# Kernel optimization log

Measured on AMD Instinct MI355X. Metric: run time of the kernel, lower is better.

Reference implementation:

```python
import jax, jax.numpy as jnp
import numpy as np

N_NODES = 100000
N_EDGES = 800000
IN_SIZE = 128
OUT_SIZE = 64
DEPTH = 2


def setup_inputs() -> dict:
    key = jax.random.key(0)
    k1, k2, k3, k4, k5 = jax.random.split(key, 5)
    data = jax.random.normal(k1, (N_NODES, IN_SIZE), dtype=jnp.float32)
    W = jax.random.normal(k2, (IN_SIZE, OUT_SIZE), dtype=jnp.float32) * (1.0 / np.sqrt(IN_SIZE))
    b = jax.random.normal(k3, (OUT_SIZE,), dtype=jnp.float32) * 0.01
    src_idx = jax.random.randint(k4, (N_EDGES,), 0, N_NODES, dtype=jnp.int64)
    tgt_idx = jnp.sort(jax.random.randint(k5, (N_EDGES,), 0, N_NODES, dtype=jnp.int64))
    return {"data": data, "W": W, "b": b, "src_idx": src_idx, "tgt_idx": tgt_idx}


def reference(data, W, b, src_idx, tgt_idx):
    # GCN(X,S) = relu( A_S^depth (X W + b) )
    out = data @ W + b  # [N, out_size]
    n = data.shape[0]
    # per-target edge counts (message_size); same every depth iteration
    counts = jax.ops.segment_sum(jnp.ones_like(tgt_idx, dtype=out.dtype), tgt_idx, num_segments=n)
    m = counts[tgt_idx][:, None]  # [E, 1], >= 1 wherever indexed
    for _ in range(DEPTH):
        # own/(m*(m+1)) summed over m edges of a node == own/(m+1);
        # plus sum of sources/(m+1): mean-style normalization
        msg = out[tgt_idx] / (m * (m + 1.0)) + out[src_idx] / (m + 1.0)
        out = jax.ops.segment_sum(msg, tgt_idx, num_segments=n)
    return jax.nn.relu(out)
```

## Files before the change

### kernel.cpp

```cpp
#include <hip/hip_runtime.h>

#define N_NODES 100000
#define N_EDGES 800000
#define IN_SIZE 128
#define OUT_SIZE 64

#define GEMM_BLOCKS 512
#define RP_BLOCKS   128
#define N_TILES     (N_NODES / 16)

typedef __attribute__((ext_vector_type(8))) short short8;
typedef __attribute__((ext_vector_type(4))) float f32x4;

__device__ __forceinline__ unsigned short f2bf(float x) {
    unsigned u = __float_as_uint(x);
    u += 0x7FFFu + ((u >> 16) & 1u);
    return (unsigned short)(u >> 16);
}
__device__ __forceinline__ unsigned pack2(float lo, float hi) {
    return (unsigned)f2bf(lo) | ((unsigned)f2bf(hi) << 16);
}
__device__ __forceinline__ float bflo(unsigned u) { return __uint_as_float(u << 16); }
__device__ __forceinline__ float bfhi(unsigned u) { return __uint_as_float(u & 0xFFFF0000u); }

__global__ __launch_bounds__(256) void gemm_rowptr_kernel(
    const float* __restrict__ data, const float* __restrict__ W,
    const float* __restrict__ b, const int* __restrict__ tgt,
    unsigned short* __restrict__ H, int* __restrict__ rowptr)
{
    if (blockIdx.x >= GEMM_BLOCKS) {
        int t = (int)(blockIdx.x - GEMM_BLOCKS) * 256 + (int)threadIdx.x;
        for (; t <= N_NODES; t += RP_BLOCKS * 256) {
            int lo = 0, hi = N_EDGES;
            while (lo < hi) {
                const int mid = (lo + hi) >> 1;
                if (tgt[mid] < t) lo = mid + 1; else hi = mid;
            }
            rowptr[t] = lo;
        }
        return;
    }

    __shared__ unsigned short Clds[4][16 * 72];

    const int tid  = threadIdx.x;
    const int lane = tid & 63;
    const int wv   = tid >> 6;
    const int quad = lane >> 4;
    const int col  = lane & 15;

    union U8 { short8 v; unsigned short u[8]; };

    short8 wb[4][4];
    #pragma unroll
    for (int kc = 0; kc < 4; ++kc) {
        #pragma unroll
        for (int nt = 0; nt < 4; ++nt) {
            U8 t;
            #pragma unroll
            for (int j = 0; j < 8; ++j) {
                const int k = kc * 32 + quad * 8 + j;
                t.u[j] = f2bf(W[k * OUT_SIZE + nt * 16 + col]);
            }
            wb[kc][nt] = t.v;
        }
    }
    float bcol[4];
    #pragma unroll
    for (int nt = 0; nt < 4; ++nt) bcol[nt] = b[nt * 16 + col];

    unsigned short* cl = Clds[wv];
    const int gw = blockIdx.x * 4 + wv;

    for (int tile = gw; tile < N_TILES; tile += GEMM_BLOCKS * 4) {
        const int r0 = tile * 16;
        const float* arow = data + (size_t)(r0 + col) * IN_SIZE + quad * 8;

        short8 af[4];
        #pragma unroll
        for (int kc = 0; kc < 4; ++kc) {
            const float4 x0 = *(const float4*)(arow + kc * 32);
            const float4 x1 = *(const float4*)(arow + kc * 32 + 4);
            U8 t;
            t.u[0] = f2bf(x0.x); t.u[1] = f2bf(x0.y);
            t.u[2] = f2bf(x0.z); t.u[3] = f2bf(x0.w);
            t.u[4] = f2bf(x1.x); t.u[5] = f2bf(x1.y);
            t.u[6] = f2bf(x1.z); t.u[7] = f2bf(x1.w);
            af[kc] = t.v;
        }

        f32x4 acc[4];
        #pragma unroll
        for (int nt = 0; nt < 4; ++nt) acc[nt] = (f32x4){0.f, 0.f, 0.f, 0.f};
        #pragma unroll
        for (int kc = 0; kc < 4; ++kc) {
            #pragma unroll
            for (int nt = 0; nt < 4; ++nt)
                acc[nt] = __builtin_amdgcn_mfma_f32_16x16x32_bf16(
                    af[kc], wb[kc][nt], acc[nt], 0, 0, 0);
        }

        #pragma unroll
        for (int nt = 0; nt < 4; ++nt) {
            #pragma unroll
            for (int r = 0; r < 4; ++r)
                cl[(quad * 4 + r) * 72 + nt * 16 + col] =
                    f2bf(acc[nt][r] + bcol[nt]);
        }
        #pragma unroll
        for (int p = 0; p < 2; ++p) {
            const int row = p * 8 + (lane >> 3);
            const int seg = lane & 7;
            const uint4 vv = *(const uint4*)(cl + row * 72 + seg * 8);
            *(uint4*)(H + (size_t)(r0 + row) * OUT_SIZE + seg * 8) = vv;
        }
    }
}

__device__ __forceinline__ void acc_add(float* a, const uint4 v) {
    a[0] += bflo(v.x); a[1] += bfhi(v.x);
    a[2] += bflo(v.y); a[3] += bfhi(v.y);
    a[4] += bflo(v.z); a[5] += bfhi(v.z);
    a[6] += bflo(v.w); a[7] += bfhi(v.w);
}
__device__ __forceinline__ void acc_fma(float* a, const uint4 v, const float m) {
    a[0] = fmaf(bflo(v.x), m, a[0]); a[1] = fmaf(bfhi(v.x), m, a[1]);
    a[2] = fmaf(bflo(v.y), m, a[2]); a[3] = fmaf(bfhi(v.y), m, a[3]);
    a[4] = fmaf(bflo(v.z), m, a[4]); a[5] = fmaf(bfhi(v.z), m, a[5]);
    a[6] = fmaf(bflo(v.w), m, a[6]); a[7] = fmaf(bfhi(v.w), m, a[7]);
}

template <bool FINAL>
__global__ __launch_bounds__(256) void prop_kernel(
    const unsigned short* __restrict__ in, void* __restrict__ outp,
    const int* __restrict__ rowptr, const int* __restrict__ src)
{
    const int tid   = threadIdx.x;
    const int lane  = tid & 63;
    const int s     = lane & 7;
    const int lbase = lane & 56;
    const int node  = blockIdx.x * 32 + (tid >> 3);

    const int start = rowptr[node];
    const int end   = rowptr[node + 1];
    const int deg   = end - start;

    const uint4* inq = (const uint4*)in;
    const uint4 ownq = inq[(size_t)node * 8 + s];

    float acc[8];
    #pragma unroll
    for (int k = 0; k < 8; ++k) acc[k] = 0.f;

    for (int base = start; base < end; base += 8) {
        const int li = base + s;
        const int sv = (li < end) ? src[li] : 0;
        int cm = end - base; cm = cm < 8 ? cm : 8;
        #pragma unroll
        for (int j0 = 0; j0 < 8; j0 += 4) {
            if (j0 < cm) {
                const int s0 = __shfl(sv, lbase + j0 + 0, 64);
                const int s1 = __shfl(sv, lbase + j0 + 1, 64);
                const int s2 = __shfl(sv, lbase + j0 + 2, 64);
                const int s3 = __shfl(sv, lbase + j0 + 3, 64);
                const float m1 = (j0 + 1 < cm) ? 1.f : 0.f;
                const float m2 = (j0 + 2 < cm) ? 1.f : 0.f;
                const float m3 = (j0 + 3 < cm) ? 1.f : 0.f;
                const uint4 v0 = inq[(size_t)s0 * 8 + s];
                const uint4 v1 = inq[(size_t)s1 * 8 + s];
                const uint4 v2 = inq[(size_t)s2 * 8 + s];
                const uint4 v3 = inq[(size_t)s3 * 8 + s];
                acc_add(acc, v0);
                acc_fma(acc, v1, m1);
                acc_fma(acc, v2, m2);
                acc_fma(acc, v3, m3);
            }
        }
    }

    float o[8];
    if (deg == 0) {
        #pragma unroll
        for (int k = 0; k < 8; ++k) o[k] = 0.f;
    } else {
        const float inv = 1.0f / (float)(deg + 1);
        float own[8];
        acc_add(acc, ownq);
        #pragma unroll
        for (int k = 0; k < 8; ++k) {
            o[k] = acc[k] * inv;
            if (FINAL) o[k] = fmaxf(o[k], 0.f);
        }
        (void)own;
    }

    if (FINAL) {
        float* out = (float*)outp;
        float4 lo, hi;
        lo.x = o[0]; lo.y = o[1]; lo.z = o[2]; lo.w = o[3];
        hi.x = o[4]; hi.y = o[5]; hi.z = o[6]; hi.w = o[7];
        *(float4*)(out + (size_t)node * OUT_SIZE + s * 8)     = lo;
        *(float4*)(out + (size_t)node * OUT_SIZE + s * 8 + 4) = hi;
    } else {
        uint4 pv;
        pv.x = pack2(o[0], o[1]);
        pv.y = pack2(o[2], o[3]);
        pv.z = pack2(o[4], o[5]);
        pv.w = pack2(o[6], o[7]);
        ((uint4*)outp)[(size_t)node * 8 + s] = pv;
    }
}

extern "C" void kernel_launch(void* const* d_in, const int* in_sizes, int n_in,
                              void* d_out, int out_size, void* d_ws, size_t ws_size,
                              hipStream_t stream)
{
    const float* data = (const float*)d_in[0];
    const float* W    = (const float*)d_in[1];
    const float* b    = (const float*)d_in[2];
    const int*   src  = (const int*)d_in[3];
    const int*   tgt  = (const int*)d_in[4];

    unsigned short* H0 = (unsigned short*)d_ws;
    unsigned short* H1 = H0 + (size_t)N_NODES * OUT_SIZE;
    int* rowptr        = (int*)(H1 + (size_t)N_NODES * OUT_SIZE);

    gemm_rowptr_kernel<<<GEMM_BLOCKS + RP_BLOCKS, 256, 0, stream>>>(
        data, W, b, tgt, H0, rowptr);
    prop_kernel<false><<<N_NODES / 32, 256, 0, stream>>>(H0, H1, rowptr, src);
    prop_kernel<true ><<<N_NODES / 32, 256, 0, stream>>>(H1, d_out, rowptr, src);
}
```

Baseline: 152.2 us.

## Split bf16 feature matrix into column planes for cache-friendly gather

```diff
diff --git a/kernel.cpp b/kernel.cpp
--- a/kernel.cpp
+++ b/kernel.cpp
@@ -8,6 +8,9 @@
 #define GEMM_BLOCKS 512
 #define RP_BLOCKS   128
 #define N_TILES     (N_NODES / 16)
+
+#define PROP_CHUNKS 782
+#define PROP_BLOCKS (8 * 391)
 
 typedef __attribute__((ext_vector_type(8))) short short8;
 typedef __attribute__((ext_vector_type(4))) float f32x4;
@@ -71,6 +74,7 @@
 
     unsigned short* cl = Clds[wv];
     const int gw = blockIdx.x * 4 + wv;
+    uint4* Hq = (uint4*)H;
 
     for (int tile = gw; tile < N_TILES; tile += GEMM_BLOCKS * 4) {
         const int r0 = tile * 16;
@@ -112,22 +116,23 @@
             const int row = p * 8 + (lane >> 3);
             const int seg = lane & 7;
             const uint4 vv = *(const uint4*)(cl + row * 72 + seg * 8);
-            *(uint4*)(H + (size_t)(r0 + row) * OUT_SIZE + seg * 8) = vv;
-        }
-    }
-}
-
-__device__ __forceinline__ void acc_add(float* a, const uint4 v) {
+            Hq[(size_t)(seg >> 1) * (N_NODES * 2) +
+               (size_t)(r0 + row) * 2 + (seg & 1)] = vv;
+        }
+    }
+}
+
+__device__ __forceinline__ void acc_fma8(float* a, const uint4 v, const float m) {
+    a[0] = fmaf(bflo(v.x), m, a[0]); a[1] = fmaf(bfhi(v.x), m, a[1]);
+    a[2] = fmaf(bflo(v.y), m, a[2]); a[3] = fmaf(bfhi(v.y), m, a[3]);
+    a[4] = fmaf(bflo(v.z), m, a[4]); a[5] = fmaf(bfhi(v.z), m, a[5]);
+    a[6] = fmaf(bflo(v.w), m, a[6]); a[7] = fmaf(bfhi(v.w), m, a[7]);
+}
+__device__ __forceinline__ void acc_add8(float* a, const uint4 v) {
     a[0] += bflo(v.x); a[1] += bfhi(v.x);
     a[2] += bflo(v.y); a[3] += bfhi(v.y);
     a[4] += bflo(v.z); a[5] += bfhi(v.z);
     a[6] += bflo(v.w); a[7] += bfhi(v.w);
-}
-__device__ __forceinline__ void acc_fma(float* a, const uint4 v, const float m) {
-    a[0] = fmaf(bflo(v.x), m, a[0]); a[1] = fmaf(bfhi(v.x), m, a[1]);
-    a[2] = fmaf(bflo(v.y), m, a[2]); a[3] = fmaf(bfhi(v.y), m, a[3]);
-    a[4] = fmaf(bflo(v.z), m, a[4]); a[5] = fmaf(bfhi(v.z), m, a[5]);
-    a[6] = fmaf(bflo(v.w), m, a[6]); a[7] = fmaf(bfhi(v.w), m, a[7]);
 }
 
 template <bool FINAL>
@@ -136,46 +141,45 @@
     const int* __restrict__ rowptr, const int* __restrict__ src)
 {
     const int tid   = threadIdx.x;
-    const int lane  = tid & 63;
-    const int s     = lane & 7;
-    const int lbase = lane & 56;
-    const int node  = blockIdx.x * 32 + (tid >> 3);
+    const int oct   = blockIdx.x & 7;
+    const int q     = oct >> 1;
+    const int chunk = ((int)blockIdx.x >> 3) * 2 + (oct & 1);
+    const int s     = tid & 1;
+    const int noder = chunk * 128 + (tid >> 1);
+    const bool valid = noder < N_NODES;
+    const int node  = valid ? noder : N_NODES - 1;
 
     const int start = rowptr[node];
     const int end   = rowptr[node + 1];
     const int deg   = end - start;
 
-    const uint4* inq = (const uint4*)in;
-    const uint4 ownq = inq[(size_t)node * 8 + s];
-
-    float acc[8];
+    const uint4* plane = (const uint4*)in + (size_t)q * (N_NODES * 2);
+    const uint4 ownq = plane[(size_t)node * 2 + s];
+
+    float acc0[8], acc1[8];
     #pragma unroll
-    for (int k = 0; k < 8; ++k) acc[k] = 0.f;
-
-    for (int base = start; base < end; base += 8) {
-        const int li = base + s;
-        const int sv = (li < end) ? src[li] : 0;
-        int cm = end - base; cm = cm < 8 ? cm : 8;
-        #pragma unroll
-        for (int j0 = 0; j0 < 8; j0 += 4) {
-            if (j0 < cm) {
-                const int s0 = __shfl(sv, lbase + j0 + 0, 64);
-                const int s1 = __shfl(sv, lbase + j0 + 1, 64);
-                const int s2 = __shfl(sv, lbase + j0 + 2, 64);
-                const int s3 = __shfl(sv, lbase + j0 + 3, 64);
-                const float m1 = (j0 + 1 < cm) ? 1.f : 0.f;
-                const float m2 = (j0 + 2 < cm) ? 1.f : 0.f;
-                const float m3 = (j0 + 3 < cm) ? 1.f : 0.f;
-                const uint4 v0 = inq[(size_t)s0 * 8 + s];
-                const uint4 v1 = inq[(size_t)s1 * 8 + s];
-                const uint4 v2 = inq[(size_t)s2 * 8 + s];
-                const uint4 v3 = inq[(size_t)s3 * 8 + s];
-                acc_add(acc, v0);
-                acc_fma(acc, v1, m1);
-                acc_fma(acc, v2, m2);
-                acc_fma(acc, v3, m3);
-            }
-        }
+    for (int k = 0; k < 8; ++k) { acc0[k] = 0.f; acc1[k] = 0.f; }
+
+    for (int e = start; e < end; e += 4) {
+        const int cm = end - e;
+        const int i1 = e + (cm > 1 ? 1 : 0);
+        const int i2 = e + (cm > 2 ? 2 : 0);
+        const int i3 = e + (cm > 3 ? 3 : 0);
+        const int s0 = src[e];
+        const int s1 = src[i1];
+        const int s2 = src[i2];
+        const int s3 = src[i3];
+        const uint4 v0 = plane[(size_t)s0 * 2 + s];
+        const uint4 v1 = plane[(size_t)s1 * 2 + s];
+        const uint4 v2 = plane[(size_t)s2 * 2 + s];
+        const uint4 v3 = plane[(size_t)s3 * 2 + s];
+        const float m1 = cm > 1 ? 1.f : 0.f;
+        const float m2 = cm > 2 ? 1.f : 0.f;
+        const float m3 = cm > 3 ? 1.f : 0.f;
+        acc_add8(acc0, v0);
+        acc_fma8(acc1, v1, m1);
+        acc_fma8(acc0, v2, m2);
+        acc_fma8(acc1, v3, m3);
     }
 
     float o[8];
@@ -183,31 +187,31 @@
         #pragma unroll
         for (int k = 0; k < 8; ++k) o[k] = 0.f;
     } else {
+        acc_add8(acc0, ownq);
         const float inv = 1.0f / (float)(deg + 1);
-        float own[8];
-        acc_add(acc, ownq);
         #pragma unroll
         for (int k = 0; k < 8; ++k) {
-            o[k] = acc[k] * inv;
+            o[k] = (acc0[k] + acc1[k]) * inv;
             if (FINAL) o[k] = fmaxf(o[k], 0.f);
         }
-        (void)own;
-    }
+    }
+
+    if (!valid) return;
 
     if (FINAL) {
-        float* out = (float*)outp;
+        float* out = (float*)outp + (size_t)node * OUT_SIZE + q * 16 + s * 8;
         float4 lo, hi;
         lo.x = o[0]; lo.y = o[1]; lo.z = o[2]; lo.w = o[3];
         hi.x = o[4]; hi.y = o[5]; hi.z = o[6]; hi.w = o[7];
-        *(float4*)(out + (size_t)node * OUT_SIZE + s * 8)     = lo;
-        *(float4*)(out + (size_t)node * OUT_SIZE + s * 8 + 4) = hi;
+        *(float4*)out       = lo;
+        *(float4*)(out + 4) = hi;
     } else {
         uint4 pv;
         pv.x = pack2(o[0], o[1]);
         pv.y = pack2(o[2], o[3]);
         pv.z = pack2(o[4], o[5]);
         pv.w = pack2(o[6], o[7]);
-        ((uint4*)outp)[(size_t)node * 8 + s] = pv;
+        ((uint4*)outp)[(size_t)q * (N_NODES * 2) + (size_t)node * 2 + s] = pv;
     }
 }
 
@@ -227,6 +231,6 @@
 
     gemm_rowptr_kernel<<<GEMM_BLOCKS + RP_BLOCKS, 256, 0, stream>>>(
         data, W, b, tgt, H0, rowptr);
-    prop_kernel<false><<<N_NODES / 32, 256, 0, stream>>>(H0, H1, rowptr, src);
-    prop_kernel<true ><<<N_NODES / 32, 256, 0, stream>>>(H1, d_out, rowptr, src);
-}
+    prop_kernel<false><<<PROP_BLOCKS, 256, 0, stream>>>(H0, H1, rowptr, src);
+    prop_kernel<true ><<<PROP_BLOCKS, 256, 0, stream>>>(H1, d_out, rowptr, src);
+}
```

Result: slower. 170.5 us (+12.0%).

## Quantize intermediate node features to per-row int8 with scale to halve gather bytes

Applied to the files above, without the earlier changes.

```diff
diff --git a/kernel.cpp b/kernel.cpp
--- a/kernel.cpp
+++ b/kernel.cpp
@@ -8,6 +8,7 @@
 #define GEMM_BLOCKS 512
 #define RP_BLOCKS   128
 #define N_TILES     (N_NODES / 16)
+#define PROP_BLOCKS ((N_NODES + 63) / 64)
 
 typedef __attribute__((ext_vector_type(8))) short short8;
 typedef __attribute__((ext_vector_type(4))) float f32x4;
@@ -17,16 +18,12 @@
     u += 0x7FFFu + ((u >> 16) & 1u);
     return (unsigned short)(u >> 16);
 }
-__device__ __forceinline__ unsigned pack2(float lo, float hi) {
-    return (unsigned)f2bf(lo) | ((unsigned)f2bf(hi) << 16);
-}
-__device__ __forceinline__ float bflo(unsigned u) { return __uint_as_float(u << 16); }
-__device__ __forceinline__ float bfhi(unsigned u) { return __uint_as_float(u & 0xFFFF0000u); }
+
 
 __global__ __launch_bounds__(256) void gemm_rowptr_kernel(
     const float* __restrict__ data, const float* __restrict__ W,
     const float* __restrict__ b, const int* __restrict__ tgt,
-    unsigned short* __restrict__ H, int* __restrict__ rowptr)
+    uint4* __restrict__ H, float* __restrict__ Hs, int* __restrict__ rowptr)
 {
     if (blockIdx.x >= GEMM_BLOCKS) {
         int t = (int)(blockIdx.x - GEMM_BLOCKS) * 256 + (int)threadIdx.x;
@@ -41,7 +38,7 @@
         return;
     }
 
-    __shared__ unsigned short Clds[4][16 * 72];
+    __shared__ unsigned Clds[4][16 * 20];
 
     const int tid  = threadIdx.x;
     const int lane = tid & 63;
@@ -69,7 +66,7 @@
     #pragma unroll
     for (int nt = 0; nt < 4; ++nt) bcol[nt] = b[nt * 16 + col];
 
-    unsigned short* cl = Clds[wv];
+    unsigned* cl = Clds[wv];
     const int gw = blockIdx.x * 4 + wv;
 
     for (int tile = gw; tile < N_TILES; tile += GEMM_BLOCKS * 4) {
@@ -100,114 +97,196 @@
                     af[kc], wb[kc][nt], acc[nt], 0, 0, 0);
         }
 
-        #pragma unroll
-        for (int nt = 0; nt < 4; ++nt) {
+        float v[4][4];
+        #pragma unroll
+        for (int nt = 0; nt < 4; ++nt)
             #pragma unroll
             for (int r = 0; r < 4; ++r)
-                cl[(quad * 4 + r) * 72 + nt * 16 + col] =
-                    f2bf(acc[nt][r] + bcol[nt]);
-        }
-        #pragma unroll
-        for (int p = 0; p < 2; ++p) {
-            const int row = p * 8 + (lane >> 3);
-            const int seg = lane & 7;
-            const uint4 vv = *(const uint4*)(cl + row * 72 + seg * 8);
-            *(uint4*)(H + (size_t)(r0 + row) * OUT_SIZE + seg * 8) = vv;
+                v[nt][r] = acc[nt][r] + bcol[nt];
+
+        float rmax[4];
+        #pragma unroll
+        for (int r = 0; r < 4; ++r) {
+            float m = fabsf(v[0][r]);
+            m = fmaxf(m, fabsf(v[1][r]));
+            m = fmaxf(m, fabsf(v[2][r]));
+            m = fmaxf(m, fabsf(v[3][r]));
+            m = fmaxf(m, __shfl_xor(m, 1, 64));
+            m = fmaxf(m, __shfl_xor(m, 2, 64));
+            m = fmaxf(m, __shfl_xor(m, 4, 64));
+            m = fmaxf(m, __shfl_xor(m, 8, 64));
+            rmax[r] = m;
+        }
+        if (col < 4)
+            Hs[r0 + quad * 4 + col] = rmax[col] * (1.f / 127.f);
+
+        #pragma unroll
+        for (int r = 0; r < 4; ++r) {
+            const float inv = rmax[r] > 0.f ? 127.f / rmax[r] : 0.f;
+            const unsigned u0 = (unsigned)(int)rintf(v[0][r] * inv + 128.f);
+            const unsigned u1 = (unsigned)(int)rintf(v[1][r] * inv + 128.f);
+            const unsigned u2 = (unsigned)(int)rintf(v[2][r] * inv + 128.f);
+            const unsigned u3 = (unsigned)(int)rintf(v[3][r] * inv + 128.f);
+            cl[(quad * 4 + r) * 20 + col] =
+                u0 | (u1 << 8) | (u2 << 16) | (u3 << 24);
+        }
+
+        {
+            const int row = lane >> 2;
+            const int seg = lane & 3;
+            const uint4 vv = *(const uint4*)(cl + row * 20 + seg * 4);
+            H[(size_t)(r0 + row) * 4 + seg] = vv;
         }
     }
 }
 
-__device__ __forceinline__ void acc_add(float* a, const uint4 v) {
-    a[0] += bflo(v.x); a[1] += bfhi(v.x);
-    a[2] += bflo(v.y); a[3] += bfhi(v.y);
-    a[4] += bflo(v.z); a[5] += bfhi(v.z);
-    a[6] += bflo(v.w); a[7] += bfhi(v.w);
-}
-__device__ __forceinline__ void acc_fma(float* a, const uint4 v, const float m) {
-    a[0] = fmaf(bflo(v.x), m, a[0]); a[1] = fmaf(bfhi(v.x), m, a[1]);
-    a[2] = fmaf(bflo(v.y), m, a[2]); a[3] = fmaf(bfhi(v.y), m, a[3]);
-    a[4] = fmaf(bflo(v.z), m, a[4]); a[5] = fmaf(bfhi(v.z), m, a[5]);
-    a[6] = fmaf(bflo(v.w), m, a[6]); a[7] = fmaf(bfhi(v.w), m, a[7]);
-}
+#define ACC16(vv, c)                                                        \
+    {                                                                        \
+        const unsigned* _w = (const unsigned*)&(vv);                         \
+        _Pragma("unroll")                                                    \
+        for (int _d = 0; _d < 4; ++_d) {                                     \
+            _Pragma("unroll")                                                \
+            for (int _b = 0; _b < 4; ++_b)                                   \
+                acc[_d * 4 + _b] = fmaf(                                     \
+                    (float)((_w[_d] >> (8 * _b)) & 255u), (c), acc[_d*4+_b]);\
+        }                                                                    \
+    }
 
 template <bool FINAL>
 __global__ __launch_bounds__(256) void prop_kernel(
-    const unsigned short* __restrict__ in, void* __restrict__ outp,
+    const uint4* __restrict__ inq, const float* __restrict__ insc,
+    void* __restrict__ outp, float* __restrict__ outsc,
     const int* __restrict__ rowptr, const int* __restrict__ src)
 {
     const int tid   = threadIdx.x;
     const int lane  = tid & 63;
-    const int s     = lane & 7;
-    const int lbase = lane & 56;
-    const int node  = blockIdx.x * 32 + (tid >> 3);
+    const int s     = lane & 3;
+    const int lbase = lane & 60;
+    const int noder = blockIdx.x * 64 + (tid >> 2);
+    const bool valid = noder < N_NODES;
+    const int node  = valid ? noder : N_NODES - 1;
 
     const int start = rowptr[node];
     const int end   = rowptr[node + 1];
     const int deg   = end - start;
 
-    const uint4* inq = (const uint4*)in;
-    const uint4 ownq = inq[(size_t)node * 8 + s];
-
-    float acc[8];
+    const uint4 ownq = inq[(size_t)node * 4 + s];
+    const float owns = insc[node];
+
+    float acc[16];
     #pragma unroll
-    for (int k = 0; k < 8; ++k) acc[k] = 0.f;
-
-    for (int base = start; base < end; base += 8) {
-        const int li = base + s;
-        const int sv = (li < end) ? src[li] : 0;
-        int cm = end - base; cm = cm < 8 ? cm : 8;
-        #pragma unroll
-        for (int j0 = 0; j0 < 8; j0 += 4) {
-            if (j0 < cm) {
-                const int s0 = __shfl(sv, lbase + j0 + 0, 64);
-                const int s1 = __shfl(sv, lbase + j0 + 1, 64);
-                const int s2 = __shfl(sv, lbase + j0 + 2, 64);
-                const int s3 = __shfl(sv, lbase + j0 + 3, 64);
-                const float m1 = (j0 + 1 < cm) ? 1.f : 0.f;
-                const float m2 = (j0 + 2 < cm) ? 1.f : 0.f;
-                const float m3 = (j0 + 3 < cm) ? 1.f : 0.f;
-                const uint4 v0 = inq[(size_t)s0 * 8 + s];
-                const uint4 v1 = inq[(size_t)s1 * 8 + s];
-                const uint4 v2 = inq[(size_t)s2 * 8 + s];
-                const uint4 v3 = inq[(size_t)s3 * 8 + s];
-                acc_add(acc, v0);
-                acc_fma(acc, v1, m1);
-                acc_fma(acc, v2, m2);
-                acc_fma(acc, v3, m3);
+    for (int k = 0; k < 16; ++k) acc[k] = 0.f;
+    float sumS = 0.f;
+
+    if (deg > 0) {
+        for (int base = start; base < end; base += 8) {
+            const int rem = end - base;
+            const int liA = base + s;
+            const int svA = src[liA < end ? liA : base];
+            int svB = 0;
+            if (base + 4 < end) {
+                const int liB = base + 4 + s;
+                svB = src[liB < end ? liB : base + 4];
             }
-        }
-    }
-
-    float o[8];
+            const int e0 = __shfl(svA, lbase + 0, 64);
+            const int e1 = __shfl(svA, lbase + 1, 64);
+            const int e2 = __shfl(svA, lbase + 2, 64);
+            const int e3 = __shfl(svA, lbase + 3, 64);
+            const int e4 = __shfl(svB, lbase + 0, 64);
+            const int e5 = __shfl(svB, lbase + 1, 64);
+            const int e6 = __shfl(svB, lbase + 2, 64);
+            const int e7 = __shfl(svB, lbase + 3, 64);
+
+            const int i1 = rem > 1 ? e1 : e0;
+            const int i2 = rem > 2 ? e2 : e0;
+            const int i3 = rem > 3 ? e3 : e0;
+            const int i4 = rem > 4 ? e4 : e0;
+            const int i5 = rem > 5 ? e5 : e0;
+            const int i6 = rem > 6 ? e6 : e0;
+            const int i7 = rem > 7 ? e7 : e0;
+
+            const uint4 v0 = inq[(size_t)e0 * 4 + s];
+            const uint4 v1 = inq[(size_t)i1 * 4 + s];
+            const uint4 v2 = inq[(size_t)i2 * 4 + s];
+            const uint4 v3 = inq[(size_t)i3 * 4 + s];
+            const uint4 v4 = inq[(size_t)i4 * 4 + s];
+            const uint4 v5 = inq[(size_t)i5 * 4 + s];
+            const uint4 v6 = inq[(size_t)i6 * 4 + s];
+            const uint4 v7 = inq[(size_t)i7 * 4 + s];
+
+            const float c0 = insc[e0];
+            const float c1 = rem > 1 ? insc[i1] : 0.f;
+            const float c2 = rem > 2 ? insc[i2] : 0.f;
+            const float c3 = rem > 3 ? insc[i3] : 0.f;
+            const float c4 = rem > 4 ? insc[i4] : 0.f;
+            const float c5 = rem > 5 ? insc[i5] : 0.f;
+            const float c6 = rem > 6 ? insc[i6] : 0.f;
+            const float c7 = rem > 7 ? insc[i7] : 0.f;
+
+            sumS += c0 + c1 + c2 + c3 + c4 + c5 + c6 + c7;
+            ACC16(v0, c0); ACC16(v1, c1); ACC16(v2, c2); ACC16(v3, c3);
+            ACC16(v4, c4); ACC16(v5, c5); ACC16(v6, c6); ACC16(v7, c7);
+        }
+        ACC16(ownq, owns);
+        sumS += owns;
+    }
+
+    float val[16];
     if (deg == 0) {
         #pragma unroll
-        for (int k = 0; k < 8; ++k) o[k] = 0.f;
+        for (int k = 0; k < 16; ++k) val[k] = 0.f;
     } else {
-        const float inv = 1.0f / (float)(deg + 1);
-        float own[8];
-        acc_add(acc, ownq);
-        #pragma unroll
-        for (int k = 0; k < 8; ++k) {
-            o[k] = acc[k] * inv;
-            if (FINAL) o[k] = fmaxf(o[k], 0.f);
-        }
-        (void)own;
+        const float invm  = 1.0f / (float)(deg + 1);
+        const float bias  = 128.f * sumS;
+        #pragma unroll
+        for (int k = 0; k < 16; ++k) {
+            val[k] = (acc[k] - bias) * invm;
+            if (FINAL) val[k] = fmaxf(val[k], 0.f);
+        }
     }
 
     if (FINAL) {
+        __shared__ float T[64 * 68];
+        const int nl = tid >> 2;
+        #pragma unroll
+        for (int d = 0; d < 4; ++d)
+            #pragma unroll
+            for (int bb = 0; bb < 4; ++bb)
+                T[nl * 68 + (s * 4 + d) + 16 * bb] = val[d * 4 + bb];
+        __syncthreads();
         float* out = (float*)outp;
-        float4 lo, hi;
-        lo.x = o[0]; lo.y = o[1]; lo.z = o[2]; lo.w = o[3];
-        hi.x = o[4]; hi.y = o[5]; hi.z = o[6]; hi.w = o[7];
-        *(float4*)(out + (size_t)node * OUT_SIZE + s * 8)     = lo;
-        *(float4*)(out + (size_t)node * OUT_SIZE + s * 8 + 4) = hi;
+        const int nb = blockIdx.x * 64;
+        #pragma unroll
+        for (int p = 0; p < 4; ++p) {
+            const int pos = p * 1024 + tid * 4;
+            const int n   = pos >> 6;
+            const int ch  = pos & 63;
+            if (nb + n < N_NODES) {
+                const float4 vv = *(const float4*)(T + n * 68 + ch);
+                *(float4*)(out + (size_t)(nb + n) * OUT_SIZE + ch) = vv;
+            }
+        }
     } else {
+        float m = 0.f;
+        #pragma unroll
+        for (int k = 0; k < 16; ++k) m = fmaxf(m, fabsf(val[k]));
+        m = fmaxf(m, __shfl_xor(m, 1, 64));
+        m = fmaxf(m, __shfl_xor(m, 2, 64));
+        const float invq = m > 0.f ? 127.f / m : 0.f;
         uint4 pv;
-        pv.x = pack2(o[0], o[1]);
-        pv.y = pack2(o[2], o[3]);
-        pv.z = pack2(o[4], o[5]);
-        pv.w = pack2(o[6], o[7]);
-        ((uint4*)outp)[(size_t)node * 8 + s] = pv;
+        unsigned* pw = (unsigned*)&pv;
+        #pragma unroll
+        for (int d = 0; d < 4; ++d) {
+            const unsigned u0 = (unsigned)(int)rintf(val[d * 4 + 0] * invq + 128.f);
+            const unsigned u1 = (unsigned)(int)rintf(val[d * 4 + 1] * invq + 128.f);
+            const unsigned u2 = (unsigned)(int)rintf(val[d * 4 + 2] * invq + 128.f);
+            const unsigned u3 = (unsigned)(int)rintf(val[d * 4 + 3] * invq + 128.f);
+            pw[d] = u0 | (u1 << 8) | (u2 << 16) | (u3 << 24);
+        }
+        if (valid) {
+            ((uint4*)outp)[(size_t)node * 4 + s] = pv;
+            if (s == 0) outsc[node] = m * (1.f / 127.f);
+        }
     }
 }
 
@@ -221,12 +300,17 @@
     const int*   src  = (const int*)d_in[3];
     const int*   tgt  = (const int*)d_in[4];
 
-    unsigned short* H0 = (unsigned short*)d_ws;
-    unsigned short* H1 = H0 + (size_t)N_NODES * OUT_SIZE;
-    int* rowptr        = (int*)(H1 + (size_t)N_NODES * OUT_SIZE);
+    char*  base   = (char*)d_ws;
+    uint4* H0     = (uint4*)base;
+    uint4* H1     = (uint4*)(base + (size_t)N_NODES * OUT_SIZE);
+    float* H0s    = (float*)(base + 2 * (size_t)N_NODES * OUT_SIZE);
+    float* H1s    = H0s + N_NODES;
+    int*   rowptr = (int*)(H1s + N_NODES);
 
     gemm_rowptr_kernel<<<GEMM_BLOCKS + RP_BLOCKS, 256, 0, stream>>>(
-        data, W, b, tgt, H0, rowptr);
-    prop_kernel<false><<<N_NODES / 32, 256, 0, stream>>>(H0, H1, rowptr, src);
-    prop_kernel<true ><<<N_NODES / 32, 256, 0, stream>>>(H1, d_out, rowptr, src);
+        data, W, b, tgt, H0, H0s, rowptr);
+    prop_kernel<false><<<PROP_BLOCKS, 256, 0, stream>>>(
+        H0, H0s, (void*)H1, H1s, rowptr, src);
+    prop_kernel<true ><<<PROP_BLOCKS, 256, 0, stream>>>(
+        H1, H1s, d_out, nullptr, rowptr, src);
 }
```

Result: no change. 149.8 us (-1.6%).
